# Kernel tuning notes

Hardware: AMD Instinct MI355X
Metric: run time of the kernel (lower is better)

Reference implementation:

```python
import jax, jax.numpy as jnp
import numpy as np

DIM = 1024
HEADS = 16
HEAD_DIM = DIM // HEADS
THETA = 10000.0


def _freqs_cis(d, n, theta=THETA):
    # complex rotary frequencies, shape (n, d//2)
    pos = jnp.arange(n, dtype=jnp.float32)
    inv = 1.0 / theta ** (jnp.arange(0, d, 2, dtype=jnp.float32) / d)
    ang = jnp.outer(pos, inv)
    return jax.lax.complex(jnp.cos(ang), jnp.sin(ang))


def _to_complex(x):
    # (..., d) -> (..., d//2) complex via adjacent pairs
    xr = x.astype(jnp.float32).reshape(*x.shape[:-1], -1, 2)
    return jax.lax.complex(xr[..., 0], xr[..., 1])


def _to_real(xc):
    # (..., d//2) complex -> (..., d) interleaved real/imag
    return jnp.stack([jnp.real(xc), jnp.imag(xc)], axis=-1).reshape(*xc.shape[:-1], -1)


def setup_inputs() -> dict:
    key = jax.random.key(0)
    k1, k2, k3 = jax.random.split(key, 3)
    b, seq = 2, 2048
    x = jax.random.normal(k1, (b, DIM, seq), dtype=jnp.float32)
    w_qkv = jax.random.normal(k2, (3 * DIM, DIM), dtype=jnp.float32) * (DIM ** -0.5)
    w_out = jax.random.normal(k3, (DIM, DIM), dtype=jnp.float32) * (DIM ** -0.5)
    return {"x": x, "w_qkv": w_qkv, "w_out": w_out}


def reference(x, w_qkv, w_out):
    b, dim, n = x.shape
    h, hd = HEADS, HEAD_DIM
    scale = hd ** -0.5
    xt = jnp.swapaxes(x, -1, -2)                      # (b, t, dim)
    qkv = jnp.einsum('btd,ed->bte', xt, w_qkv)        # (b, t, 3*dim)
    q, k, v = jnp.split(qkv, 3, axis=-1)
    q = q.reshape(b, n, h, hd)
    k = k.reshape(b, n, h, hd)
    v = v.reshape(b, n, h, hd)
    # rotary embedding on q, k
    fc = _freqs_cis(hd, n)[None, :, None, :]          # (1, t, 1, hd//2)
    q = _to_real(_to_complex(q) * fc).astype(x.dtype)
    k = _to_real(_to_complex(k) * fc).astype(x.dtype)
    # naive full attention
    logits = jnp.einsum('bqhd,bkhd->bhqk', q, k) * scale
    probs = jax.nn.softmax(logits, axis=-1)
    out = jnp.einsum('bhqk,bkhd->bqhd', probs, v)     # (b, t, h, hd)
    out = out.reshape(b, n, dim)
    out = jnp.einsum('btd,ed->bte', out, w_out)       # (b, t, dim)
    return jnp.swapaxes(out, -1, -2)                  # (b, dim, t)
```

## Files before the change

### kernel.cpp

```cpp
#include <hip/hip_runtime.h>
#include <hip/hip_bf16.h>
#include <math.h>

#define B 2
#define N 2048
#define D 1024
#define H 16
#define HD 64

typedef __attribute__((ext_vector_type(8))) short short8;
typedef __attribute__((ext_vector_type(4))) float f32x4;
typedef __attribute__((ext_vector_type(16))) float f32x16;
typedef __attribute__((ext_vector_type(4))) unsigned short ush4;
typedef __attribute__((ext_vector_type(4))) unsigned int uint4v;

__device__ __forceinline__ float bf2f(unsigned short u) {
  unsigned int x = ((unsigned int)u) << 16;
  float f;
  __builtin_memcpy(&f, &x, 4);
  return f;
}
__device__ __forceinline__ unsigned short f2bf(float f) {
  unsigned int x;
  __builtin_memcpy(&x, &f, 4);
  x = x + 0x7fffu + ((x >> 16) & 1u);
  return (unsigned short)(x >> 16);
}
__device__ __forceinline__ unsigned int pk2(float lo, float hi) {
  union { __hip_bfloat162 h; unsigned int u; } cv;
  cv.h = __float22bfloat162_rn(make_float2(lo, hi));
  return cv.u;
}
__device__ __forceinline__ short8 mk_frag(unsigned int w0, unsigned int w1,
                                          unsigned int w2, unsigned int w3) {
  union { uint4v u; short8 s; } cv;
  cv.u = (uint4v){w0, w1, w2, w3};
  return cv.s;
}

__device__ __forceinline__ void gload16(const unsigned short* g, unsigned short* l) {
  __builtin_amdgcn_global_load_lds(
      (const __attribute__((address_space(1))) unsigned int*)(const void*)g,
      (__attribute__((address_space(3))) unsigned int*)(void*)l, 16, 0, 0);
}

__global__ void prep_k(const float* __restrict__ wqkv, unsigned short* __restrict__ wqkv_bf,
                       const float* __restrict__ wout, unsigned short* __restrict__ wout_bf,
                       float2* __restrict__ tab) {
  int blk = blockIdx.x;
  if (blk < 4096) {
    const float* src = (blk < 3072) ? wqkv : wout;
    unsigned short* dst = (blk < 3072) ? wqkv_bf : wout_bf;
    int i = (blk < 3072 ? blk : blk - 3072) * 256 + threadIdx.x;
    float4 v = ((const float4*)src)[i];
    ush4 o;
    o[0] = f2bf(v.x); o[1] = f2bf(v.y); o[2] = f2bf(v.z); o[3] = f2bf(v.w);
    *(ush4*)&dst[i * 4] = o;
  } else {
    int idx = (blk - 4096) * 256 + threadIdx.x;
    int t = idx >> 5, p = idx & 31;
    float inv = powf(10000.f, -(float)p / 32.f);
    float ang = (float)t * inv;
    float s, c;
    sincosf(ang, &s, &c);
    tab[idx] = make_float2(c, s);
  }
}

__global__ __launch_bounds__(256) void transpose_x(const float* __restrict__ x,
                                                   unsigned short* __restrict__ xt) {
  __shared__ float tile[32][33];
  const int tx = threadIdx.x, ty = threadIdx.y;
  const int t0 = blockIdx.x * 32, d0 = blockIdx.y * 32, bb = blockIdx.z;
#pragma unroll
  for (int i = 0; i < 4; ++i) {
    int r = ty * 4 + i;
    tile[r][tx] = x[(size_t)bb * D * N + (size_t)(d0 + r) * N + t0 + tx];
  }
  __syncthreads();
#pragma unroll
  for (int i = 0; i < 4; ++i) {
    int r = ty * 4 + i;
    xt[((size_t)(bb * N) + t0 + r) * D + d0 + tx] = f2bf(tile[tx][r]);
  }
}

template <int MODE>
__global__ __launch_bounds__(256) void gemm_bt(const unsigned short* __restrict__ A,
                                               const unsigned short* __restrict__ Bt,
                                               float* __restrict__ outf,
                                               unsigned short* __restrict__ qkbuf,
                                               unsigned short* __restrict__ vtbuf) {
  __shared__ unsigned short Asm[128 * 64];
  __shared__ unsigned short Bsm[128 * 64];
  const int tid = threadIdx.x;
  const int lane = tid & 63, wid = tid >> 6;
  const int ln = lane & 15, lh = lane >> 4;
  const int wr = wid >> 1, wc = wid & 1;
  const int bid = blockIdx.x;
  const int xcd = bid & 7, j = bid >> 3;
  const int m0 = (xcd * 4 + (j & 3)) * 128;
  const int n0 = (j >> 2) * 128;

  f32x4 acc[4][4];
#pragma unroll
  for (int i = 0; i < 4; ++i)
#pragma unroll
    for (int jq = 0; jq < 4; ++jq) acc[i][jq] = (f32x4){0.f, 0.f, 0.f, 0.f};

  for (int k0 = 0; k0 < 1024; k0 += 64) {
#pragma unroll
    for (int jj = 0; jj < 4; ++jj) {
      int slot = tid + jj * 256;
      int row = slot >> 3, u = slot & 7;
      int usw = (u ^ (row & 7)) * 8;
      gload16(&A[(size_t)(m0 + row) * 1024 + k0 + usw], &Asm[slot * 8]);
    }
#pragma unroll
    for (int jj = 0; jj < 4; ++jj) {
      int slot = tid + jj * 256;
      int row = slot >> 3, u = slot & 7;
      int usw = (u ^ (row & 7)) * 8;
      gload16(&Bt[(size_t)(n0 + row) * 1024 + k0 + usw], &Bsm[slot * 8]);
    }
    __syncthreads();
#pragma unroll
    for (int s = 0; s < 2; ++s) {
      short8 af[4], bfr[4];
#pragma unroll
      for (int i = 0; i < 4; ++i) {
        int row = wr * 64 + i * 16 + ln;
        int u = ((s * 4 + lh) ^ (row & 7)) * 8;
        af[i] = *(const short8*)&Asm[row * 64 + u];
      }
#pragma unroll
      for (int jq = 0; jq < 4; ++jq) {
        int row = wc * 64 + jq * 16 + ln;
        int u = ((s * 4 + lh) ^ (row & 7)) * 8;
        bfr[jq] = *(const short8*)&Bsm[row * 64 + u];
      }
#pragma unroll
      for (int i = 0; i < 4; ++i)
#pragma unroll
        for (int jq = 0; jq < 4; ++jq)
          acc[i][jq] = __builtin_amdgcn_mfma_f32_16x16x32_bf16(af[i], bfr[jq], acc[i][jq], 0, 0, 0);
    }
    __syncthreads();
  }

#pragma unroll
  for (int i = 0; i < 4; ++i) {
    int mrow = m0 + wr * 64 + i * 16 + lh * 4;
    int bb = mrow >> 11, t = mrow & 2047;
#pragma unroll
    for (int jq = 0; jq < 4; ++jq) {
      int e = n0 + wc * 64 + jq * 16 + ln;
      if (MODE == 1) {
        float* op = outf + (size_t)bb * D * N + (size_t)e * N + t;
        *(f32x4*)op = acc[i][jq];
      } else {
        if (e < 2048) {
#pragma unroll
          for (int jj = 0; jj < 4; ++jj)
            qkbuf[((size_t)(bb * N + t + jj)) * 2048 + e] = f2bf(acc[i][jq][jj]);
        } else {
          ush4 v;
#pragma unroll
          for (int jj = 0; jj < 4; ++jj) v[jj] = f2bf(acc[i][jq][jj]);
          *(ush4*)&vtbuf[((size_t)bb * 1024 + (e - 2048)) * N + t] = v;
        }
      }
    }
  }
}

__global__ void rope_kernel(unsigned short* __restrict__ qk, const float2* __restrict__ tab) {
  int idx = blockIdx.x * 256 + threadIdx.x;
  int e = (idx & 255) * 8;
  int t = (idx >> 8) & 2047;
  int bb = idx >> 19;
  int p0 = (e & 63) >> 1;
  const float qscl = 0.125f * 1.4426950408889634f;
  float sc = (e < 1024) ? qscl : 1.0f;
  unsigned short* p = qk + ((size_t)(bb * N + t)) * 2048 + e;
  short8 v = *(short8*)p;
#pragma unroll
  for (int q = 0; q < 4; ++q) {
    float2 cs = tab[t * 32 + p0 + q];
    float xe = bf2f((unsigned short)v[2 * q]);
    float xo = bf2f((unsigned short)v[2 * q + 1]);
    v[2 * q] = (short)f2bf((xe * cs.x - xo * cs.y) * sc);
    v[2 * q + 1] = (short)f2bf((xe * cs.y + xo * cs.x) * sc);
  }
  *(short8*)p = v;
}

__global__ __launch_bounds__(256, 2) void attn_kernel(const unsigned short* __restrict__ qk,
                                                      const unsigned short* __restrict__ vt,
                                                      unsigned short* __restrict__ ob) {
  __shared__ unsigned short Ksm[2][64 * 64];
  __shared__ unsigned short Vsm[2][64 * 64];
  const int tid = threadIdx.x;
  const int lane = tid & 63, wid = tid >> 6;
  const int l31 = lane & 31, hi = lane >> 5;
  const int L = blockIdx.x;
  const int hh = L & 31, qb = L >> 5;
  const int bb = hh >> 4, h = hh & 15;
  const unsigned short* Qg = qk + (size_t)bb * N * 2048 + h * 64;
  const unsigned short* Kg = Qg + 1024;
  const unsigned short* Vg = vt + ((size_t)bb * 1024 + h * 64) * N;

  const int q = qb * 128 + wid * 32 + l31;
  short8 qf[4];
#pragma unroll
  for (int c = 0; c < 4; ++c)
    qf[c] = *(const short8*)&Qg[(size_t)q * 2048 + c * 16 + hi * 8];

  f32x16 oL, oH;
#pragma unroll
  for (int r = 0; r < 16; ++r) { oL[r] = 0.f; oH[r] = 0.f; }
  float lrun = 0.f;

  auto STAGE = [&](int buf, int kb) {
#pragma unroll
    for (int jj = 0; jj < 2; ++jj) {
      int slot = tid + jj * 256;
      int row = slot >> 3, u = slot & 7;
      int usw = (u ^ (row & 7)) * 8;
      gload16(&Kg[(size_t)(kb + row) * 2048 + usw], &Ksm[buf][slot * 8]);
    }
#pragma unroll
    for (int jj = 0; jj < 2; ++jj) {
      int slot = tid + jj * 256;
      int row = slot >> 3, u = slot & 7;
      int usw = (u ^ (row & 7)) * 8;
      gload16(&Vg[(size_t)row * N + kb + usw], &Vsm[buf][slot * 8]);
    }
  };

  STAGE(0, 0);
  __syncthreads();
  int cur = 0;
  for (int t = 0; t < N / 64; ++t) {
    if (t < N / 64 - 1) STAGE(cur ^ 1, (t + 1) * 64);
    f32x16 s0, s1;
#pragma unroll
    for (int r = 0; r < 16; ++r) { s0[r] = 0.f; s1[r] = 0.f; }
    __builtin_amdgcn_s_setprio(1);
#pragma unroll
    for (int c = 0; c < 4; ++c) {
      short8 ka = *(const short8*)&Ksm[cur][l31 * 64 + (((c * 2 + hi) ^ (l31 & 7)) * 8)];
      s0 = __builtin_amdgcn_mfma_f32_32x32x16_bf16(ka, qf[c], s0, 0, 0, 0);
      int r1 = 32 + l31;
      short8 kb2 = *(const short8*)&Ksm[cur][r1 * 64 + (((c * 2 + hi) ^ (r1 & 7)) * 8)];
      s1 = __builtin_amdgcn_mfma_f32_32x32x16_bf16(kb2, qf[c], s1, 0, 0, 0);
    }
    __builtin_amdgcn_s_setprio(0);
    float lsum = 0.f;
#pragma unroll
    for (int r = 0; r < 16; ++r) {
      s0[r] = __builtin_amdgcn_exp2f(s0[r]);
      s1[r] = __builtin_amdgcn_exp2f(s1[r]);
      lsum += s0[r] + s1[r];
    }
    lrun += lsum;
    unsigned int W[16];
#pragma unroll
    for (int i = 0; i < 8; ++i) {
      W[i] = pk2(s0[2 * i], s0[2 * i + 1]);
      W[8 + i] = pk2(s1[2 * i], s1[2 * i + 1]);
    }
    short8 pf[4];
#pragma unroll
    for (int c = 0; c < 4; ++c) {
      unsigned int a0 = W[4 * c + 0], b0 = W[4 * c + 2];
      unsigned int a1 = W[4 * c + 1], b1 = W[4 * c + 3];
      asm volatile("v_permlane32_swap_b32 %0, %1" : "+v"(a0), "+v"(b0));
      asm volatile("v_permlane32_swap_b32 %0, %1" : "+v"(a1), "+v"(b1));
      pf[c] = mk_frag(a0, a1, b0, b1);
    }
    __builtin_amdgcn_s_setprio(1);
#pragma unroll
    for (int c = 0; c < 4; ++c) {
      short8 va = *(const short8*)&Vsm[cur][l31 * 64 + (((c * 2 + hi) ^ (l31 & 7)) * 8)];
      oL = __builtin_amdgcn_mfma_f32_32x32x16_bf16(va, pf[c], oL, 0, 0, 0);
      int rH = 32 + l31;
      short8 vb = *(const short8*)&Vsm[cur][rH * 64 + (((c * 2 + hi) ^ (rH & 7)) * 8)];
      oH = __builtin_amdgcn_mfma_f32_32x32x16_bf16(vb, pf[c], oH, 0, 0, 0);
    }
    __builtin_amdgcn_s_setprio(0);
    __syncthreads();
    cur ^= 1;
  }
  lrun += __shfl_xor(lrun, 32, 64);
  float inv = 1.f / lrun;
  unsigned short* obp = ob + ((size_t)(bb * N + q)) * 1024 + h * 64;
#pragma unroll
  for (int r4 = 0; r4 < 4; ++r4) {
    ush4 vL, vH;
#pragma unroll
    for (int i = 0; i < 4; ++i) {
      vL[i] = f2bf(oL[r4 * 4 + i] * inv);
      vH[i] = f2bf(oH[r4 * 4 + i] * inv);
    }
    *(ush4*)&obp[r4 * 8 + hi * 4] = vL;
    *(ush4*)&obp[32 + r4 * 8 + hi * 4] = vH;
  }
}

extern "C" void kernel_launch(void* const* d_in, const int* in_sizes, int n_in,
                              void* d_out, int out_size, void* d_ws, size_t ws_size,
                              hipStream_t stream) {
  const float* x = (const float*)d_in[0];
  const float* w_qkv = (const float*)d_in[1];
  const float* w_out = (const float*)d_in[2];
  float* out = (float*)d_out;
  char* ws = (char*)d_ws;

  unsigned short* wqkv_bf = (unsigned short*)ws;
  unsigned short* wout_bf = (unsigned short*)(ws + 6291456);
  unsigned short* xt      = (unsigned short*)(ws + 8388608);
  unsigned short* qkbuf   = (unsigned short*)(ws + 16777216);
  unsigned short* vtbuf   = (unsigned short*)(ws + 33554432);
  float2* tab             = (float2*)(ws + 41943040);

  prep_k<<<4352, 256, 0, stream>>>(w_qkv, wqkv_bf, w_out, wout_bf, tab);
  transpose_x<<<dim3(N / 32, D / 32, B), dim3(32, 8), 0, stream>>>(x, xt);

  gemm_bt<0><<<768, 256, 0, stream>>>(xt, wqkv_bf, nullptr, qkbuf, vtbuf);
  rope_kernel<<<4096, 256, 0, stream>>>(qkbuf, tab);
  attn_kernel<<<512, 256, 0, stream>>>(qkbuf, vtbuf, xt );
  gemm_bt<1><<<256, 256, 0, stream>>>(xt, wout_bf, out, nullptr, nullptr);
}
```

Before: 127.2 us.

## Fuse Q rotary into attention and double KV tile to 128 with split-barrier pipeline

The rope kernel now rotates only K, and attention applies rotary plus softmax scale to Q as it loads it into registers, which halves the rope kernel's traffic. The attention loop now stages 128-key K/V tiles, so there are half as many iterations. It replaces __syncthreads with explicit barriers and vmcnt waits so the next tile's loads overlap compute. This doubles LDS use per block, which may limit occupancy, and relies on the hand-written waitcnt counts being correct.

```diff
diff --git a/kernel.cpp b/kernel.cpp
--- a/kernel.cpp
+++ b/kernel.cpp
@@ -176,12 +176,10 @@
 
 __global__ void rope_kernel(unsigned short* __restrict__ qk, const float2* __restrict__ tab) {
   int idx = blockIdx.x * 256 + threadIdx.x;
-  int e = (idx & 255) * 8;
-  int t = (idx >> 8) & 2047;
-  int bb = idx >> 19;
+  int e = 1024 + (idx & 127) * 8;
+  int t = (idx >> 7) & 2047;
+  int bb = idx >> 18;
   int p0 = (e & 63) >> 1;
-  const float qscl = 0.125f * 1.4426950408889634f;
-  float sc = (e < 1024) ? qscl : 1.0f;
   unsigned short* p = qk + ((size_t)(bb * N + t)) * 2048 + e;
   short8 v = *(short8*)p;
 #pragma unroll
@@ -189,17 +187,18 @@
     float2 cs = tab[t * 32 + p0 + q];
     float xe = bf2f((unsigned short)v[2 * q]);
     float xo = bf2f((unsigned short)v[2 * q + 1]);
-    v[2 * q] = (short)f2bf((xe * cs.x - xo * cs.y) * sc);
-    v[2 * q + 1] = (short)f2bf((xe * cs.y + xo * cs.x) * sc);
+    v[2 * q] = (short)f2bf(xe * cs.x - xo * cs.y);
+    v[2 * q + 1] = (short)f2bf(xe * cs.y + xo * cs.x);
   }
   *(short8*)p = v;
 }
 
 __global__ __launch_bounds__(256, 2) void attn_kernel(const unsigned short* __restrict__ qk,
                                                       const unsigned short* __restrict__ vt,
-                                                      unsigned short* __restrict__ ob) {
-  __shared__ unsigned short Ksm[2][64 * 64];
-  __shared__ unsigned short Vsm[2][64 * 64];
+                                                      unsigned short* __restrict__ ob,
+                                                      const float2* __restrict__ tab) {
+  __shared__ unsigned short Ksm[2][128 * 64];
+  __shared__ unsigned short Vsm[2][64 * 128];
   const int tid = threadIdx.x;
   const int lane = tid & 63, wid = tid >> 6;
   const int l31 = lane & 31, hi = lane >> 5;
@@ -211,51 +210,62 @@
   const unsigned short* Vg = vt + ((size_t)bb * 1024 + h * 64) * N;
 
   const int q = qb * 128 + wid * 32 + l31;
+  const float qscl = 0.125f * 1.4426950408889634f;
   short8 qf[4];
 #pragma unroll
-  for (int c = 0; c < 4; ++c)
-    qf[c] = *(const short8*)&Qg[(size_t)q * 2048 + c * 16 + hi * 8];
-
-  f32x16 oL, oH;
-#pragma unroll
-  for (int r = 0; r < 16; ++r) { oL[r] = 0.f; oH[r] = 0.f; }
+  for (int c = 0; c < 4; ++c) {
+    short8 raw = *(const short8*)&Qg[(size_t)q * 2048 + c * 16 + hi * 8];
+    short8 f;
+#pragma unroll
+    for (int pp = 0; pp < 4; ++pp) {
+      float2 cs = tab[q * 32 + c * 8 + hi * 4 + pp];
+      float xe = bf2f((unsigned short)raw[2 * pp]);
+      float xo = bf2f((unsigned short)raw[2 * pp + 1]);
+      f[2 * pp] = (short)f2bf((xe * cs.x - xo * cs.y) * qscl);
+      f[2 * pp + 1] = (short)f2bf((xe * cs.y + xo * cs.x) * qscl);
+    }
+    qf[c] = f;
+  }
+
+  f32x16 z16;
+#pragma unroll
+  for (int r = 0; r < 16; ++r) z16[r] = 0.f;
+  f32x16 oL = z16, oH = z16;
   float lrun = 0.f;
 
   auto STAGE = [&](int buf, int kb) {
 #pragma unroll
-    for (int jj = 0; jj < 2; ++jj) {
+    for (int jj = 0; jj < 4; ++jj) {
       int slot = tid + jj * 256;
       int row = slot >> 3, u = slot & 7;
       int usw = (u ^ (row & 7)) * 8;
       gload16(&Kg[(size_t)(kb + row) * 2048 + usw], &Ksm[buf][slot * 8]);
     }
 #pragma unroll
-    for (int jj = 0; jj < 2; ++jj) {
+    for (int jj = 0; jj < 4; ++jj) {
       int slot = tid + jj * 256;
-      int row = slot >> 3, u = slot & 7;
-      int usw = (u ^ (row & 7)) * 8;
+      int row = slot >> 4, u = slot & 15;
+      int usw = (u ^ (row & 15)) * 8;
       gload16(&Vg[(size_t)row * N + kb + usw], &Vsm[buf][slot * 8]);
     }
   };
 
-  STAGE(0, 0);
-  __syncthreads();
-  int cur = 0;
-  for (int t = 0; t < N / 64; ++t) {
-    if (t < N / 64 - 1) STAGE(cur ^ 1, (t + 1) * 64);
+  auto COMPUTE64 = [&](const unsigned short* Kb, const unsigned short* Vb, int h2) {
+    const int r0 = h2 * 64 + l31, r1 = h2 * 64 + 32 + l31;
     f32x16 s0, s1;
-#pragma unroll
-    for (int r = 0; r < 16; ++r) { s0[r] = 0.f; s1[r] = 0.f; }
-    __builtin_amdgcn_s_setprio(1);
-#pragma unroll
-    for (int c = 0; c < 4; ++c) {
-      short8 ka = *(const short8*)&Ksm[cur][l31 * 64 + (((c * 2 + hi) ^ (l31 & 7)) * 8)];
+    {
+      short8 ka = *(const short8*)&Kb[r0 * 64 + (((0 + hi) ^ (r0 & 7)) * 8)];
+      s0 = __builtin_amdgcn_mfma_f32_32x32x16_bf16(ka, qf[0], z16, 0, 0, 0);
+      short8 kc = *(const short8*)&Kb[r1 * 64 + (((0 + hi) ^ (r1 & 7)) * 8)];
+      s1 = __builtin_amdgcn_mfma_f32_32x32x16_bf16(kc, qf[0], z16, 0, 0, 0);
+    }
+#pragma unroll
+    for (int c = 1; c < 4; ++c) {
+      short8 ka = *(const short8*)&Kb[r0 * 64 + (((c * 2 + hi) ^ (r0 & 7)) * 8)];
       s0 = __builtin_amdgcn_mfma_f32_32x32x16_bf16(ka, qf[c], s0, 0, 0, 0);
-      int r1 = 32 + l31;
-      short8 kb2 = *(const short8*)&Ksm[cur][r1 * 64 + (((c * 2 + hi) ^ (r1 & 7)) * 8)];
-      s1 = __builtin_amdgcn_mfma_f32_32x32x16_bf16(kb2, qf[c], s1, 0, 0, 0);
-    }
-    __builtin_amdgcn_s_setprio(0);
+      short8 kc = *(const short8*)&Kb[r1 * 64 + (((c * 2 + hi) ^ (r1 & 7)) * 8)];
+      s1 = __builtin_amdgcn_mfma_f32_32x32x16_bf16(kc, qf[c], s1, 0, 0, 0);
+    }
     float lsum = 0.f;
 #pragma unroll
     for (int r = 0; r < 16; ++r) {
@@ -279,19 +289,38 @@
       asm volatile("v_permlane32_swap_b32 %0, %1" : "+v"(a1), "+v"(b1));
       pf[c] = mk_frag(a0, a1, b0, b1);
     }
+    const int vA = l31, vB = 32 + l31;
+#pragma unroll
+    for (int c = 0; c < 4; ++c) {
+      int ua = ((h2 * 8 + c * 2 + hi) ^ (vA & 15)) * 8;
+      short8 va = *(const short8*)&Vb[vA * 128 + ua];
+      oL = __builtin_amdgcn_mfma_f32_32x32x16_bf16(va, pf[c], oL, 0, 0, 0);
+      int ub = ((h2 * 8 + c * 2 + hi) ^ (vB & 15)) * 8;
+      short8 vb = *(const short8*)&Vb[vB * 128 + ub];
+      oH = __builtin_amdgcn_mfma_f32_32x32x16_bf16(vb, pf[c], oH, 0, 0, 0);
+    }
+  };
+
+  STAGE(0, 0);
+  int cur = 0;
+  for (int t = 0; t < 16; ++t) {
+    __builtin_amdgcn_sched_barrier(0);
+    __builtin_amdgcn_s_barrier();
+    if (t < 15) {
+      STAGE(cur ^ 1, (t + 1) * 128);
+      asm volatile("s_waitcnt vmcnt(8)" ::: "memory");
+    } else {
+      asm volatile("s_waitcnt vmcnt(0)" ::: "memory");
+    }
+    __builtin_amdgcn_sched_barrier(0);
+    __builtin_amdgcn_s_barrier();
     __builtin_amdgcn_s_setprio(1);
-#pragma unroll
-    for (int c = 0; c < 4; ++c) {
-      short8 va = *(const short8*)&Vsm[cur][l31 * 64 + (((c * 2 + hi) ^ (l31 & 7)) * 8)];
-      oL = __builtin_amdgcn_mfma_f32_32x32x16_bf16(va, pf[c], oL, 0, 0, 0);
-      int rH = 32 + l31;
-      short8 vb = *(const short8*)&Vsm[cur][rH * 64 + (((c * 2 + hi) ^ (rH & 7)) * 8)];
-      oH = __builtin_amdgcn_mfma_f32_32x32x16_bf16(vb, pf[c], oH, 0, 0, 0);
-    }
+    COMPUTE64(Ksm[cur], Vsm[cur], 0);
+    COMPUTE64(Ksm[cur], Vsm[cur], 1);
     __builtin_amdgcn_s_setprio(0);
-    __syncthreads();
     cur ^= 1;
   }
+
   lrun += __shfl_xor(lrun, 32, 64);
   float inv = 1.f / lrun;
   unsigned short* obp = ob + ((size_t)(bb * N + q)) * 1024 + h * 64;
@@ -328,7 +357,7 @@
   transpose_x<<<dim3(N / 32, D / 32, B), dim3(32, 8), 0, stream>>>(x, xt);
 
   gemm_bt<0><<<768, 256, 0, stream>>>(xt, wqkv_bf, nullptr, qkbuf, vtbuf);
-  rope_kernel<<<4096, 256, 0, stream>>>(qkbuf, tab);
-  attn_kernel<<<512, 256, 0, stream>>>(qkbuf, vtbuf, xt );
+  rope_kernel<<<2048, 256, 0, stream>>>(qkbuf, tab);
+  attn_kernel<<<512, 256, 0, stream>>>(qkbuf, vtbuf, xt , tab);
   gemm_bt<1><<<256, 256, 0, stream>>>(xt, wout_bf, out, nullptr, nullptr);
 }
```

After: 126.6 us. About the same (-0.5%).

## Split attention over two key halves and fuse Q rotary into attention

Applied to the files above, without the earlier changes.

The attention kernel now splits the key range into two halves across separate blocks, doubling the grid to 1024 blocks, and writes unnormalized partial outputs plus row sums. A new combine kernel merges and normalizes them, using the output buffer as scratch. Rotary embedding and scaling for Q move into the attention kernel's Q load, so the rope kernel only processes K. The launch bound asks for 4 blocks per CU. The intent is better occupancy and parallelism, paid for by an extra kernel, extra partial-output traffic, and bf16 rounding of the partials. The softmax uses no running max, so adding partials is exact in form.

```diff
diff --git a/kernel.cpp b/kernel.cpp
--- a/kernel.cpp
+++ b/kernel.cpp
@@ -9,6 +9,7 @@
 #define HD 64
 
 typedef __attribute__((ext_vector_type(8))) short short8;
+typedef __attribute__((ext_vector_type(8))) unsigned short ush8;
 typedef __attribute__((ext_vector_type(4))) float f32x4;
 typedef __attribute__((ext_vector_type(16))) float f32x16;
 typedef __attribute__((ext_vector_type(4))) unsigned short ush4;
@@ -176,12 +177,10 @@
 
 __global__ void rope_kernel(unsigned short* __restrict__ qk, const float2* __restrict__ tab) {
   int idx = blockIdx.x * 256 + threadIdx.x;
-  int e = (idx & 255) * 8;
-  int t = (idx >> 8) & 2047;
-  int bb = idx >> 19;
+  int e = 1024 + (idx & 127) * 8;
+  int t = (idx >> 7) & 2047;
+  int bb = idx >> 18;
   int p0 = (e & 63) >> 1;
-  const float qscl = 0.125f * 1.4426950408889634f;
-  float sc = (e < 1024) ? qscl : 1.0f;
   unsigned short* p = qk + ((size_t)(bb * N + t)) * 2048 + e;
   short8 v = *(short8*)p;
 #pragma unroll
@@ -189,32 +188,47 @@
     float2 cs = tab[t * 32 + p0 + q];
     float xe = bf2f((unsigned short)v[2 * q]);
     float xo = bf2f((unsigned short)v[2 * q + 1]);
-    v[2 * q] = (short)f2bf((xe * cs.x - xo * cs.y) * sc);
-    v[2 * q + 1] = (short)f2bf((xe * cs.y + xo * cs.x) * sc);
+    v[2 * q] = (short)f2bf(xe * cs.x - xo * cs.y);
+    v[2 * q + 1] = (short)f2bf(xe * cs.y + xo * cs.x);
   }
   *(short8*)p = v;
 }
 
-__global__ __launch_bounds__(256, 2) void attn_kernel(const unsigned short* __restrict__ qk,
+__global__ __launch_bounds__(256, 4) void attn_kernel(const unsigned short* __restrict__ qk,
                                                       const unsigned short* __restrict__ vt,
-                                                      unsigned short* __restrict__ ob) {
+                                                      unsigned short* __restrict__ O0,
+                                                      unsigned short* __restrict__ O1,
+                                                      float* __restrict__ lp,
+                                                      const float2* __restrict__ tab) {
   __shared__ unsigned short Ksm[2][64 * 64];
   __shared__ unsigned short Vsm[2][64 * 64];
   const int tid = threadIdx.x;
   const int lane = tid & 63, wid = tid >> 6;
   const int l31 = lane & 31, hi = lane >> 5;
   const int L = blockIdx.x;
-  const int hh = L & 31, qb = L >> 5;
+  const int hh = L & 31, qb = (L >> 5) & 15, s = L >> 9;
   const int bb = hh >> 4, h = hh & 15;
   const unsigned short* Qg = qk + (size_t)bb * N * 2048 + h * 64;
   const unsigned short* Kg = Qg + 1024;
   const unsigned short* Vg = vt + ((size_t)bb * 1024 + h * 64) * N;
 
   const int q = qb * 128 + wid * 32 + l31;
+  const float qscl = 0.125f * 1.4426950408889634f;
   short8 qf[4];
 #pragma unroll
-  for (int c = 0; c < 4; ++c)
-    qf[c] = *(const short8*)&Qg[(size_t)q * 2048 + c * 16 + hi * 8];
+  for (int c = 0; c < 4; ++c) {
+    short8 raw = *(const short8*)&Qg[(size_t)q * 2048 + c * 16 + hi * 8];
+    short8 f;
+#pragma unroll
+    for (int pp = 0; pp < 4; ++pp) {
+      float2 cs = tab[q * 32 + c * 8 + hi * 4 + pp];
+      float xe = bf2f((unsigned short)raw[2 * pp]);
+      float xo = bf2f((unsigned short)raw[2 * pp + 1]);
+      f[2 * pp] = (short)f2bf((xe * cs.x - xo * cs.y) * qscl);
+      f[2 * pp + 1] = (short)f2bf((xe * cs.y + xo * cs.x) * qscl);
+    }
+    qf[c] = f;
+  }
 
   f32x16 oL, oH;
 #pragma unroll
@@ -238,11 +252,12 @@
     }
   };
 
-  STAGE(0, 0);
+  const int kb0 = s * 1024;
+  STAGE(0, kb0);
   __syncthreads();
   int cur = 0;
-  for (int t = 0; t < N / 64; ++t) {
-    if (t < N / 64 - 1) STAGE(cur ^ 1, (t + 1) * 64);
+  for (int t = 0; t < 16; ++t) {
+    if (t < 15) STAGE(cur ^ 1, kb0 + (t + 1) * 64);
     f32x16 s0, s1;
 #pragma unroll
     for (int r = 0; r < 16; ++r) { s0[r] = 0.f; s1[r] = 0.f; }
@@ -293,19 +308,36 @@
     cur ^= 1;
   }
   lrun += __shfl_xor(lrun, 32, 64);
-  float inv = 1.f / lrun;
-  unsigned short* obp = ob + ((size_t)(bb * N + q)) * 1024 + h * 64;
+
+  unsigned short* obp = (s ? O1 : O0) + ((size_t)(bb * N + q)) * 1024 + h * 64;
 #pragma unroll
   for (int r4 = 0; r4 < 4; ++r4) {
     ush4 vL, vH;
 #pragma unroll
     for (int i = 0; i < 4; ++i) {
-      vL[i] = f2bf(oL[r4 * 4 + i] * inv);
-      vH[i] = f2bf(oH[r4 * 4 + i] * inv);
+      vL[i] = f2bf(oL[r4 * 4 + i]);
+      vH[i] = f2bf(oH[r4 * 4 + i]);
     }
     *(ush4*)&obp[r4 * 8 + hi * 4] = vL;
     *(ush4*)&obp[32 + r4 * 8 + hi * 4] = vH;
   }
+  if (!hi) lp[((size_t)(s * B + bb) * N + q) * H + h] = lrun;
+}
+
+__global__ __launch_bounds__(128) void combine_k(unsigned short* __restrict__ O0ob,
+                                                 const unsigned short* __restrict__ O1,
+                                                 const float* __restrict__ lp) {
+  const int row = blockIdx.x;
+  const int d0 = threadIdx.x * 8;
+  const int h = d0 >> 6;
+  float l = lp[(size_t)row * H + h] + lp[(size_t)(B * N + row) * H + h];
+  float inv = 1.f / l;
+  ush8 a = *(const ush8*)&O0ob[(size_t)row * 1024 + d0];
+  ush8 b = *(const ush8*)&O1[(size_t)row * 1024 + d0];
+  ush8 r;
+#pragma unroll
+  for (int i = 0; i < 8; ++i) r[i] = f2bf((bf2f(a[i]) + bf2f(b[i])) * inv);
+  *(ush8*)&O0ob[(size_t)row * 1024 + d0] = r;
 }
 
 extern "C" void kernel_launch(void* const* d_in, const int* in_sizes, int n_in,
@@ -323,12 +355,15 @@
   unsigned short* qkbuf   = (unsigned short*)(ws + 16777216);
   unsigned short* vtbuf   = (unsigned short*)(ws + 33554432);
   float2* tab             = (float2*)(ws + 41943040);
+  float* lp               = (float*)(ws + 42467328);
+  unsigned short* O1      = (unsigned short*)d_out;
 
   prep_k<<<4352, 256, 0, stream>>>(w_qkv, wqkv_bf, w_out, wout_bf, tab);
   transpose_x<<<dim3(N / 32, D / 32, B), dim3(32, 8), 0, stream>>>(x, xt);
 
   gemm_bt<0><<<768, 256, 0, stream>>>(xt, wqkv_bf, nullptr, qkbuf, vtbuf);
-  rope_kernel<<<4096, 256, 0, stream>>>(qkbuf, tab);
-  attn_kernel<<<512, 256, 0, stream>>>(qkbuf, vtbuf, xt );
+  rope_kernel<<<2048, 256, 0, stream>>>(qkbuf, tab);
+  attn_kernel<<<1024, 256, 0, stream>>>(qkbuf, vtbuf, xt , O1, lp, tab);
+  combine_k<<<4096, 128, 0, stream>>>(xt, O1, lp);
   gemm_bt<1><<<256, 256, 0, stream>>>(xt, wout_bf, out, nullptr, nullptr);
 }
```

New measurement: 135.2 us. 6.3% more time.

## Merge prep and transpose kernels, fuse Q rope into attention, retile output GEMM

Applied to the files above, without the earlier changes.

Folds the x transpose into the weight-conversion prep kernel, so one launch does both. Moves rotary embedding and scaling of Q into the attention kernel's Q-fragment load, which halves the standalone rope kernel to K only. Splits the output projection into its own GEMM with 64-row M tiles, giving 512 blocks instead of 256 for better CU occupancy. The trade-off is extra per-thread table lookups and math in attention setup, plus a smaller per-block reuse tile in the output GEMM.

```diff
diff --git a/kernel.cpp b/kernel.cpp
--- a/kernel.cpp
+++ b/kernel.cpp
@@ -44,53 +44,54 @@
       (__attribute__((address_space(3))) unsigned int*)(void*)l, 16, 0, 0);
 }
 
-__global__ void prep_k(const float* __restrict__ wqkv, unsigned short* __restrict__ wqkv_bf,
-                       const float* __restrict__ wout, unsigned short* __restrict__ wout_bf,
-                       float2* __restrict__ tab) {
+__global__ __launch_bounds__(256) void prep_k(const float* __restrict__ wqkv,
+                                              unsigned short* __restrict__ wqkv_bf,
+                                              const float* __restrict__ wout,
+                                              unsigned short* __restrict__ wout_bf,
+                                              float2* __restrict__ tab,
+                                              const float* __restrict__ x,
+                                              unsigned short* __restrict__ xt) {
   int blk = blockIdx.x;
+  int tid = threadIdx.x;
   if (blk < 4096) {
     const float* src = (blk < 3072) ? wqkv : wout;
     unsigned short* dst = (blk < 3072) ? wqkv_bf : wout_bf;
-    int i = (blk < 3072 ? blk : blk - 3072) * 256 + threadIdx.x;
+    int i = (blk < 3072 ? blk : blk - 3072) * 256 + tid;
     float4 v = ((const float4*)src)[i];
     ush4 o;
     o[0] = f2bf(v.x); o[1] = f2bf(v.y); o[2] = f2bf(v.z); o[3] = f2bf(v.w);
     *(ush4*)&dst[i * 4] = o;
-  } else {
-    int idx = (blk - 4096) * 256 + threadIdx.x;
+  } else if (blk < 4352) {
+    int idx = (blk - 4096) * 256 + tid;
     int t = idx >> 5, p = idx & 31;
     float inv = powf(10000.f, -(float)p / 32.f);
     float ang = (float)t * inv;
     float s, c;
     sincosf(ang, &s, &c);
     tab[idx] = make_float2(c, s);
-  }
-}
-
-__global__ __launch_bounds__(256) void transpose_x(const float* __restrict__ x,
-                                                   unsigned short* __restrict__ xt) {
-  __shared__ float tile[32][33];
-  const int tx = threadIdx.x, ty = threadIdx.y;
-  const int t0 = blockIdx.x * 32, d0 = blockIdx.y * 32, bb = blockIdx.z;
-#pragma unroll
-  for (int i = 0; i < 4; ++i) {
-    int r = ty * 4 + i;
-    tile[r][tx] = x[(size_t)bb * D * N + (size_t)(d0 + r) * N + t0 + tx];
-  }
-  __syncthreads();
-#pragma unroll
-  for (int i = 0; i < 4; ++i) {
-    int r = ty * 4 + i;
-    xt[((size_t)(bb * N) + t0 + r) * D + d0 + tx] = f2bf(tile[tx][r]);
-  }
-}
-
-template <int MODE>
-__global__ __launch_bounds__(256) void gemm_bt(const unsigned short* __restrict__ A,
-                                               const unsigned short* __restrict__ Bt,
-                                               float* __restrict__ outf,
-                                               unsigned short* __restrict__ qkbuf,
-                                               unsigned short* __restrict__ vtbuf) {
+  } else {
+    __shared__ float tile[32][33];
+    int tb = blk - 4352;
+    int t0 = (tb & 63) * 32, d0 = ((tb >> 6) & 31) * 32, bb = tb >> 11;
+    int tx = tid & 31, ty = tid >> 5;
+#pragma unroll
+    for (int i = 0; i < 4; ++i) {
+      int r = ty * 4 + i;
+      tile[r][tx] = x[(size_t)bb * D * N + (size_t)(d0 + r) * N + t0 + tx];
+    }
+    __syncthreads();
+#pragma unroll
+    for (int i = 0; i < 4; ++i) {
+      int r = ty * 4 + i;
+      xt[((size_t)(bb * N) + t0 + r) * D + d0 + tx] = f2bf(tile[tx][r]);
+    }
+  }
+}
+
+__global__ __launch_bounds__(256) void gemm_qkv(const unsigned short* __restrict__ A,
+                                                const unsigned short* __restrict__ Bt,
+                                                unsigned short* __restrict__ qkbuf,
+                                                unsigned short* __restrict__ vtbuf) {
   __shared__ unsigned short Asm[128 * 64];
   __shared__ unsigned short Bsm[128 * 64];
   const int tid = threadIdx.x;
@@ -155,33 +156,99 @@
 #pragma unroll
     for (int jq = 0; jq < 4; ++jq) {
       int e = n0 + wc * 64 + jq * 16 + ln;
-      if (MODE == 1) {
-        float* op = outf + (size_t)bb * D * N + (size_t)e * N + t;
-        *(f32x4*)op = acc[i][jq];
+      if (e < 2048) {
+#pragma unroll
+        for (int jj = 0; jj < 4; ++jj)
+          qkbuf[((size_t)(bb * N + t + jj)) * 2048 + e] = f2bf(acc[i][jq][jj]);
       } else {
-        if (e < 2048) {
-#pragma unroll
-          for (int jj = 0; jj < 4; ++jj)
-            qkbuf[((size_t)(bb * N + t + jj)) * 2048 + e] = f2bf(acc[i][jq][jj]);
-        } else {
-          ush4 v;
-#pragma unroll
-          for (int jj = 0; jj < 4; ++jj) v[jj] = f2bf(acc[i][jq][jj]);
-          *(ush4*)&vtbuf[((size_t)bb * 1024 + (e - 2048)) * N + t] = v;
-        }
+        ush4 v;
+#pragma unroll
+        for (int jj = 0; jj < 4; ++jj) v[jj] = f2bf(acc[i][jq][jj]);
+        *(ush4*)&vtbuf[((size_t)bb * 1024 + (e - 2048)) * N + t] = v;
       }
+    }
+  }
+}
+
+__global__ __launch_bounds__(256) void gemm_out(const unsigned short* __restrict__ A,
+                                                const unsigned short* __restrict__ Bt,
+                                                float* __restrict__ outf) {
+  __shared__ unsigned short Asm[64 * 64];
+  __shared__ unsigned short Bsm[128 * 64];
+  const int tid = threadIdx.x;
+  const int lane = tid & 63, wid = tid >> 6;
+  const int ln = lane & 15, lh = lane >> 4;
+  const int wr = wid >> 1, wc = wid & 1;
+  const int bid = blockIdx.x;
+  const int xcd = bid & 7, j = bid >> 3;
+  const int m0 = (xcd * 8 + (j & 7)) * 64;
+  const int n0 = (j >> 3) * 128;
+
+  f32x4 acc[2][4];
+#pragma unroll
+  for (int i = 0; i < 2; ++i)
+#pragma unroll
+    for (int jq = 0; jq < 4; ++jq) acc[i][jq] = (f32x4){0.f, 0.f, 0.f, 0.f};
+
+  for (int k0 = 0; k0 < 1024; k0 += 64) {
+#pragma unroll
+    for (int jj = 0; jj < 2; ++jj) {
+      int slot = tid + jj * 256;
+      int row = slot >> 3, u = slot & 7;
+      int usw = (u ^ (row & 7)) * 8;
+      gload16(&A[(size_t)(m0 + row) * 1024 + k0 + usw], &Asm[slot * 8]);
+    }
+#pragma unroll
+    for (int jj = 0; jj < 4; ++jj) {
+      int slot = tid + jj * 256;
+      int row = slot >> 3, u = slot & 7;
+      int usw = (u ^ (row & 7)) * 8;
+      gload16(&Bt[(size_t)(n0 + row) * 1024 + k0 + usw], &Bsm[slot * 8]);
+    }
+    __syncthreads();
+#pragma unroll
+    for (int s = 0; s < 2; ++s) {
+      short8 af[2], bfr[4];
+#pragma unroll
+      for (int i = 0; i < 2; ++i) {
+        int row = wr * 32 + i * 16 + ln;
+        int u = ((s * 4 + lh) ^ (row & 7)) * 8;
+        af[i] = *(const short8*)&Asm[row * 64 + u];
+      }
+#pragma unroll
+      for (int jq = 0; jq < 4; ++jq) {
+        int row = wc * 64 + jq * 16 + ln;
+        int u = ((s * 4 + lh) ^ (row & 7)) * 8;
+        bfr[jq] = *(const short8*)&Bsm[row * 64 + u];
+      }
+#pragma unroll
+      for (int i = 0; i < 2; ++i)
+#pragma unroll
+        for (int jq = 0; jq < 4; ++jq)
+          acc[i][jq] = __builtin_amdgcn_mfma_f32_16x16x32_bf16(af[i], bfr[jq], acc[i][jq], 0, 0, 0);
+    }
+    __syncthreads();
+  }
+
+#pragma unroll
+  for (int i = 0; i < 2; ++i) {
+    int mrow = m0 + wr * 32 + i * 16 + lh * 4;
+    int bb = mrow >> 11, t = mrow & 2047;
+#pragma unroll
+    for (int jq = 0; jq < 4; ++jq) {
+      int e = n0 + wc * 64 + jq * 16 + ln;
+      float* op = outf + (size_t)bb * D * N + (size_t)e * N + t;
+      *(f32x4*)op = acc[i][jq];
     }
   }
 }
 
 __global__ void rope_kernel(unsigned short* __restrict__ qk, const float2* __restrict__ tab) {
   int idx = blockIdx.x * 256 + threadIdx.x;
-  int e = (idx & 255) * 8;
-  int t = (idx >> 8) & 2047;
-  int bb = idx >> 19;
+  int e = 1024 + (idx & 127) * 8;
+  int t = (idx >> 7) & 2047;
+  int bb = idx >> 18;
   int p0 = (e & 63) >> 1;
-  const float qscl = 0.125f * 1.4426950408889634f;
-  float sc = (e < 1024) ? qscl : 1.0f;
   unsigned short* p = qk + ((size_t)(bb * N + t)) * 2048 + e;
   short8 v = *(short8*)p;
 #pragma unroll
@@ -189,15 +256,16 @@
     float2 cs = tab[t * 32 + p0 + q];
     float xe = bf2f((unsigned short)v[2 * q]);
     float xo = bf2f((unsigned short)v[2 * q + 1]);
-    v[2 * q] = (short)f2bf((xe * cs.x - xo * cs.y) * sc);
-    v[2 * q + 1] = (short)f2bf((xe * cs.y + xo * cs.x) * sc);
+    v[2 * q] = (short)f2bf(xe * cs.x - xo * cs.y);
+    v[2 * q + 1] = (short)f2bf(xe * cs.y + xo * cs.x);
   }
   *(short8*)p = v;
 }
 
 __global__ __launch_bounds__(256, 2) void attn_kernel(const unsigned short* __restrict__ qk,
                                                       const unsigned short* __restrict__ vt,
-                                                      unsigned short* __restrict__ ob) {
+                                                      unsigned short* __restrict__ ob,
+                                                      const float2* __restrict__ tab) {
   __shared__ unsigned short Ksm[2][64 * 64];
   __shared__ unsigned short Vsm[2][64 * 64];
   const int tid = threadIdx.x;
@@ -211,10 +279,22 @@
   const unsigned short* Vg = vt + ((size_t)bb * 1024 + h * 64) * N;
 
   const int q = qb * 128 + wid * 32 + l31;
+  const float qscl = 0.125f * 1.4426950408889634f;
   short8 qf[4];
 #pragma unroll
-  for (int c = 0; c < 4; ++c)
-    qf[c] = *(const short8*)&Qg[(size_t)q * 2048 + c * 16 + hi * 8];
+  for (int c = 0; c < 4; ++c) {
+    short8 raw = *(const short8*)&Qg[(size_t)q * 2048 + c * 16 + hi * 8];
+    short8 f;
+#pragma unroll
+    for (int pp = 0; pp < 4; ++pp) {
+      float2 cs = tab[q * 32 + c * 8 + hi * 4 + pp];
+      float xe = bf2f((unsigned short)raw[2 * pp]);
+      float xo = bf2f((unsigned short)raw[2 * pp + 1]);
+      f[2 * pp] = (short)f2bf((xe * cs.x - xo * cs.y) * qscl);
+      f[2 * pp + 1] = (short)f2bf((xe * cs.y + xo * cs.x) * qscl);
+    }
+    qf[c] = f;
+  }
 
   f32x16 oL, oH;
 #pragma unroll
@@ -324,11 +404,10 @@
   unsigned short* vtbuf   = (unsigned short*)(ws + 33554432);
   float2* tab             = (float2*)(ws + 41943040);
 
-  prep_k<<<4352, 256, 0, stream>>>(w_qkv, wqkv_bf, w_out, wout_bf, tab);
-  transpose_x<<<dim3(N / 32, D / 32, B), dim3(32, 8), 0, stream>>>(x, xt);
-
-  gemm_bt<0><<<768, 256, 0, stream>>>(xt, wqkv_bf, nullptr, qkbuf, vtbuf);
-  rope_kernel<<<4096, 256, 0, stream>>>(qkbuf, tab);
-  attn_kernel<<<512, 256, 0, stream>>>(qkbuf, vtbuf, xt );
-  gemm_bt<1><<<256, 256, 0, stream>>>(xt, wout_bf, out, nullptr, nullptr);
-}
+  prep_k<<<8448, 256, 0, stream>>>(w_qkv, wqkv_bf, w_out, wout_bf, tab, x, xt);
+
+  gemm_qkv<<<768, 256, 0, stream>>>(xt, wqkv_bf, qkbuf, vtbuf);
+  rope_kernel<<<2048, 256, 0, stream>>>(qkbuf, tab);
+  attn_kernel<<<512, 256, 0, stream>>>(qkbuf, vtbuf, xt , tab);
+  gemm_out<<<512, 256, 0, stream>>>(xt, wout_bf, out);
+}
```

New measurement: 119.4 us. 1.07x faster.
